# Kernel optimization log

Hardware: AMD Instinct MI355X
Metric: run time of the kernel (lower is better)

## Reference

```python
import jax, jax.numpy as jnp
import numpy as np

N = 50000; E = 400000; T = 300000; Q = 200000
F_IN = 128; H = 8; DIM = 32; D = H * DIM; NUM_RBF = 40
CENTERS = jnp.arange(0.0, 10.0, 0.25, dtype=jnp.float32)  # 40 RBF centers
BETA = 40.0  # 10 / gap


def _norm(v):
    return jnp.sqrt(jnp.sum(jnp.square(v), -1) + 1e-12)


def _rbf(d):  # d: [M] -> [M, NUM_RBF]
    return jnp.exp(-BETA * jnp.square(d[:, None] - CENTERS))


def _angle(a, m, b):  # angle at m
    u = a - m; v = b - m
    c = jnp.sum(u * v, -1) / (_norm(u) * _norm(v) + 1e-12)
    return jnp.arccos(jnp.clip(c, -1.0 + 1e-7, 1.0 - 1e-7))


def _dihedral(p0, p1, p2, p3):
    b1 = p1 - p0; b2 = p2 - p1; b3 = p3 - p2
    n1 = jnp.cross(b1, b2); n2 = jnp.cross(b2, b3)
    m1 = jnp.cross(n1, b2 / (_norm(b2)[:, None] + 1e-12))
    return jnp.arctan2(jnp.sum(m1 * n2, -1), jnp.sum(n1 * n2, -1) + 1e-12)


def _pos_encoding():  # sinusoidal PE over the length-4 [src,mid2,mid1,dst] sequence
    i = jnp.arange(0, D, 2, dtype=jnp.float32)
    div = jnp.exp(-jnp.log(10000.0) * i / D)
    ang = jnp.arange(4.0)[:, None] * div[None, :]
    pe = jnp.zeros((4, D), jnp.float32)
    return pe.at[:, 0::2].set(jnp.sin(ang)).at[:, 1::2].set(jnp.cos(ang))


def _seg_softmax(score, dst):  # softmax over irregular neighbor sets per dst node
    e = jnp.exp(score - score.max())  # global-max shift, as in original
    den = jax.ops.segment_sum(e, dst, num_segments=N)
    return e / (den[dst] + 1e-16)


def _forward(x, pos, W_src, W_dst, W_mid1, W_mid2, W_pos_bonded, b_pos_bonded,
             W_pos_unb, b_pos_unb, W_pos_unb1, b_pos_unb1, W_pos_unb2, b_pos_unb2,
             W_angle, b_angle, W_dihedral, b_dihedral, W_1hop, b_1hop, W_2hop, b_2hop,
             W_3hop, b_3hop, attn2, attn3, attn4, W_res, bias, ln_gamma, ln_beta,
             prelu_w, edge_index, triple_index, quadra_index, edge_attr):
    pe = _pos_encoding()
    src = (x @ W_src + pe[0]).reshape(N, H, DIM)
    mid2 = (x @ W_mid2 + pe[1]).reshape(N, H, DIM)
    mid1 = (x @ W_mid1 + pe[2]).reshape(N, H, DIM)
    dst = (x @ W_dst + pe[3]).reshape(N, H, DIM)

    # ---- 1-hop edge attention ----
    es, ed = edge_index[0], edge_index[1]
    d1 = _norm(pos[es] - pos[ed])
    d1c = jnp.clip(d1, 0.05, 10.0)
    bonded = jnp.stack([d1, d1 * d1], -1)  # [E,2]
    ea = edge_attr.astype(jnp.float32)[:, None]
    dmat = ((bonded * (1.0 - ea)) @ W_pos_bonded + b_pos_bonded
            + (_rbf(d1c) * ea) @ W_pos_unb + b_pos_unb).reshape(-1, H, DIM)
    a = jax.nn.leaky_relu((mid1[es] + dst[ed]) * dmat, 0.2)
    score = jnp.sum(attn2[None] * a, -1)  # [E,H]
    w = _seg_softmax(score, ed)[..., None]
    out1 = jax.ops.segment_sum(mid1[es] * w, ed, num_segments=N)

    # ---- 2-hop (angle) attention ----
    ts, tm, td = triple_index[0], triple_index[1], triple_index[2]
    d2 = jnp.clip(_norm(pos[ts] - pos[td]), 0.05, 10.0)
    dmat2 = (_rbf(d2) @ W_pos_unb1 + b_pos_unb1).reshape(-1, H, DIM)
    ang = _angle(pos[ts], pos[tm], pos[td])
    amat = (jnp.stack([ang, ang * ang], -1) @ W_angle + b_angle).reshape(-1, H, DIM)
    a = jax.nn.leaky_relu((mid2[ts] + dst[td] + mid1[tm]) * (amat + dmat2), 0.2)
    score = jnp.sum(attn3[None] * a, -1)
    w = _seg_softmax(score, td)[..., None]
    out2 = jax.ops.segment_sum(mid2[ts] * w, td, num_segments=N)

    # ---- 3-hop (dihedral) attention ----
    qs, q2, q1, qd = quadra_index[0], quadra_index[1], quadra_index[2], quadra_index[3]
    d3 = jnp.clip(_norm(pos[qs] - pos[qd]), 0.05, 10.0)
    dmat3 = (_rbf(d3) @ W_pos_unb2 + b_pos_unb2).reshape(-1, H, DIM)
    a1 = _angle(pos[qs], pos[q2], pos[q1])
    a2 = _angle(pos[q2], pos[q1], pos[qd])
    dh = _dihedral(pos[qs], pos[q2], pos[q1], pos[qd])
    feat = jnp.stack([a1, a1 * a1, a2, a2 * a2, dh, dh * dh], -1)  # [Q,6]
    hmat = (feat @ W_dihedral + b_dihedral).reshape(-1, H, DIM)
    a = jax.nn.leaky_relu((src[qs] + mid2[q2] + mid1[q1] + dst[qd]) * (hmat + dmat3), 0.2)
    score = jnp.sum(attn4[None] * a, -1)
    w = _seg_softmax(score, qd)[..., None]
    out3 = jax.ops.segment_sum(src[qs] * w, qd, num_segments=N)

    out = (out1.reshape(N, D) @ W_1hop + b_1hop
           + out2.reshape(N, D) @ W_2hop + b_2hop
           + out3.reshape(N, D) @ W_3hop + b_3hop)
    out = out + x @ W_res + bias  # residual + bias
    mu = jnp.mean(out, -1, keepdims=True)
    var = jnp.mean(jnp.square(out - mu), -1, keepdims=True)
    out = (out - mu) * jax.lax.rsqrt(var + 1e-5) * ln_gamma + ln_beta
    return jnp.where(out >= 0, out, prelu_w * out)  # PReLU


def setup_inputs():
    key = jax.random.key(0)
    ks = jax.random.split(key, 40)
    inp = {}
    inp['x'] = jax.random.normal(ks[0], (N, F_IN), jnp.float32)
    inp['pos'] = jax.random.normal(ks[1], (N, 3), jnp.float32) * 3.0
    inp['edge_index'] = jax.random.randint(ks[2], (2, E), 0, N)
    inp['triple_index'] = jax.random.randint(ks[3], (3, T), 0, N)
    inp['quadra_index'] = jax.random.randint(ks[4], (4, Q), 0, N)
    inp['edge_attr'] = jax.random.randint(ks[5], (E,), 0, 2).astype(bool)
    params = [('W_src', (F_IN, D)), ('W_dst', (F_IN, D)), ('W_mid1', (F_IN, D)),
              ('W_mid2', (F_IN, D)), ('W_pos_bonded', (2, D)), ('b_pos_bonded', (D,)),
              ('W_pos_unb', (NUM_RBF, D)), ('b_pos_unb', (D,)),
              ('W_pos_unb1', (NUM_RBF, D)), ('b_pos_unb1', (D,)),
              ('W_pos_unb2', (NUM_RBF, D)), ('b_pos_unb2', (D,)),
              ('W_angle', (2, D)), ('b_angle', (D,)),
              ('W_dihedral', (6, D)), ('b_dihedral', (D,)),
              ('W_1hop', (D, D)), ('b_1hop', (D,)),
              ('W_2hop', (D, D)), ('b_2hop', (D,)),
              ('W_3hop', (D, D)), ('b_3hop', (D,)),
              ('attn2', (H, DIM)), ('attn3', (H, DIM)), ('attn4', (H, DIM)),
              ('W_res', (F_IN, D)), ('bias', (D,))]
    for i, (nm, sh) in enumerate(params):
        inp[nm] = jax.random.normal(ks[6 + i], sh, jnp.float32) * 0.05
    inp['ln_gamma'] = jnp.ones((D,), jnp.float32)
    inp['ln_beta'] = jnp.zeros((D,), jnp.float32)
    inp['prelu_w'] = jnp.full((1,), 0.25, jnp.float32)
    return inp


def reference(x, pos, edge_index, triple_index, quadra_index, edge_attr,
              W_src, W_dst, W_mid1, W_mid2, W_pos_bonded, b_pos_bonded,
              W_pos_unb, b_pos_unb, W_pos_unb1, b_pos_unb1, W_pos_unb2, b_pos_unb2,
              W_angle, b_angle, W_dihedral, b_dihedral, W_1hop, b_1hop, W_2hop, b_2hop,
              W_3hop, b_3hop, attn2, attn3, attn4, W_res, bias, ln_gamma, ln_beta, prelu_w):
    return _forward(x, pos, W_src, W_dst, W_mid1, W_mid2, W_pos_bonded, b_pos_bonded,
                    W_pos_unb, b_pos_unb, W_pos_unb1, b_pos_unb1, W_pos_unb2, b_pos_unb2,
                    W_angle, b_angle, W_dihedral, b_dihedral, W_1hop, b_1hop, W_2hop, b_2hop,
                    W_3hop, b_3hop, attn2, attn3, attn4, W_res, bias, ln_gamma, ln_beta,
                    prelu_w, edge_index, triple_index, quadra_index, edge_attr)
```

## Files before the change

kernel.cpp:

```cpp
#include <hip/hip_runtime.h>

#define NN 50000
#define NE 400000
#define NT 300000
#define NQ 200000
#define DM 256
#define FIN 128
#define NRBF 40
#define BETA_RBF 40.0f
#define TOTALP 397569

#define WSWZ_N (56 * 16 * 64 * 8)

#define NPB1 8
#define NPB2 8
#define NPB3 16
#define NBT1 (NN / NPB1)
#define NBT2 (NN / NPB2)
#define NBT3 (NN / NPB3)
#define NBT (NBT1 + NBT2 + NBT3)

typedef unsigned int u32;
typedef unsigned short u16;
typedef __attribute__((ext_vector_type(8))) short bf16x8;
typedef __attribute__((ext_vector_type(4))) float f32x4;

static __device__ __forceinline__ float bf2f(u16 h) {
  return __uint_as_float(((u32)h) << 16);
}
static __device__ __forceinline__ u16 f2bf(float f) {
  u32 u = __float_as_uint(f);
  u32 r = (u + 0x7FFFu + ((u >> 16) & 1u)) >> 16;
  return (u16)r;
}
static __device__ __forceinline__ float4 ld4f(const float* p) {
  return *reinterpret_cast<const float4*>(p);
}
static __device__ __forceinline__ float ldsc(const void* p, int isf, size_t i) {
  return isf ? ((const float*)p)[i] : bf2f(((const u16*)p)[i]);
}
static __device__ __forceinline__ float lk(float t) { return t >= 0.f ? t : 0.2f * t; }
static __device__ __forceinline__ u32 f2o(float f) {
  u32 u = __float_as_uint(f);
  return (u & 0x80000000u) ? ~u : (u | 0x80000000u);
}

struct F3 { float x, y, z; };
static __device__ __forceinline__ F3 ldp(const float* pos, int i) {
  return F3{pos[3 * i], pos[3 * i + 1], pos[3 * i + 2]};
}
static __device__ __forceinline__ F3 sub3(F3 a, F3 b) { return F3{a.x - b.x, a.y - b.y, a.z - b.z}; }
static __device__ __forceinline__ float dot3(F3 a, F3 b) { return a.x * b.x + a.y * b.y + a.z * b.z; }
static __device__ __forceinline__ F3 cross3(F3 a, F3 b) {
  return F3{a.y * b.z - a.z * b.y, a.z * b.x - a.x * b.z, a.x * b.y - a.y * b.x};
}
static __device__ __forceinline__ float norm3(F3 v) { return sqrtf(dot3(v, v) + 1e-12f); }
static __device__ __forceinline__ float angle_at(F3 a, F3 m, F3 b) {
  F3 u = sub3(a, m), v = sub3(b, m);
  float c = dot3(u, v) / (norm3(u) * norm3(v) + 1e-12f);
  c = fminf(fmaxf(c, -1.f + 1e-7f), 1.f - 1e-7f);
  return acosf(c);
}
static __device__ __forceinline__ float dihedral_f(F3 p0, F3 p1, F3 p2, F3 p3) {
  F3 b1 = sub3(p1, p0), b2 = sub3(p2, p1), b3 = sub3(p3, p2);
  F3 n1 = cross3(b1, b2), n2 = cross3(b2, b3);
  float nb2 = norm3(b2) + 1e-12f;
  F3 b2n{b2.x / nb2, b2.y / nb2, b2.z / nb2};
  F3 m1 = cross3(n1, b2n);
  return atan2f(dot3(m1, n2), dot3(n1, n2) + 1e-12f);
}

static __device__ __forceinline__ int rbf_coef(float d, float* c) {
  int j = (int)floorf(d * 4.0f) - 3;
  j = (j < 0) ? 0 : ((j > NRBF - 8) ? (NRBF - 8) : j);
  float t0 = d - 0.25f * (float)j;
#pragma unroll
  for (int k = 0; k < 8; ++k) {
    float t = t0 - 0.25f * (float)k;
    c[k] = __expf(-BETA_RBF * t * t);
  }
  return j;
}

static __device__ __forceinline__ float4 rbf_apply(const float* __restrict__ base,
                                                   float4 c0, float4 c1, float4 dm) {
  float4 w;
  w = ld4f(base + 0 * DM);
  dm.x = fmaf(c0.x, w.x, dm.x); dm.y = fmaf(c0.x, w.y, dm.y);
  dm.z = fmaf(c0.x, w.z, dm.z); dm.w = fmaf(c0.x, w.w, dm.w);
  w = ld4f(base + 1 * DM);
  dm.x = fmaf(c0.y, w.x, dm.x); dm.y = fmaf(c0.y, w.y, dm.y);
  dm.z = fmaf(c0.y, w.z, dm.z); dm.w = fmaf(c0.y, w.w, dm.w);
  w = ld4f(base + 2 * DM);
  dm.x = fmaf(c0.z, w.x, dm.x); dm.y = fmaf(c0.z, w.y, dm.y);
  dm.z = fmaf(c0.z, w.z, dm.z); dm.w = fmaf(c0.z, w.w, dm.w);
  w = ld4f(base + 3 * DM);
  dm.x = fmaf(c0.w, w.x, dm.x); dm.y = fmaf(c0.w, w.y, dm.y);
  dm.z = fmaf(c0.w, w.z, dm.z); dm.w = fmaf(c0.w, w.w, dm.w);
  w = ld4f(base + 4 * DM);
  dm.x = fmaf(c1.x, w.x, dm.x); dm.y = fmaf(c1.x, w.y, dm.y);
  dm.z = fmaf(c1.x, w.z, dm.z); dm.w = fmaf(c1.x, w.w, dm.w);
  w = ld4f(base + 5 * DM);
  dm.x = fmaf(c1.y, w.x, dm.x); dm.y = fmaf(c1.y, w.y, dm.y);
  dm.z = fmaf(c1.y, w.z, dm.z); dm.w = fmaf(c1.y, w.w, dm.w);
  w = ld4f(base + 6 * DM);
  dm.x = fmaf(c1.z, w.x, dm.x); dm.y = fmaf(c1.z, w.y, dm.y);
  dm.z = fmaf(c1.z, w.z, dm.z); dm.w = fmaf(c1.z, w.w, dm.w);
  w = ld4f(base + 7 * DM);
  dm.x = fmaf(c1.w, w.x, dm.x); dm.y = fmaf(c1.w, w.y, dm.y);
  dm.z = fmaf(c1.w, w.z, dm.z); dm.w = fmaf(c1.w, w.w, dm.w);
  return dm;
}

static __device__ __forceinline__ ushort4 g512(const u16* p, int idx, int c4) {
  return *reinterpret_cast<const ushort4*>(p + (size_t)(u32)idx * DM + c4);
}
static __device__ __forceinline__ float4 cvt4(ushort4 v) {
  return float4{bf2f(v.x), bf2f(v.y), bf2f(v.z), bf2f(v.w)};
}

__device__ const int g_off[31] = {
  0, 32768, 65536, 98304, 131072, 131584, 131840, 142080, 142336, 152576,
  152832, 163072, 163328, 163840, 164096, 165632, 165888, 231424, 231680,
  297216, 297472, 363008, 363264, 363520, 363776, 364032, 396800, 397056,
  397312, 397568, 397569};
struct PtrTab { const void* p[30]; };

__global__ __launch_bounds__(256) void init_detect(const u32* __restrict__ aw,
                                                   const u32* __restrict__ lng,
                                                   u32* __restrict__ gmax,
                                                   int* __restrict__ flags) {
  __shared__ int s_int, s_f32, s_bf;
  if (threadIdx.x == 0) { s_int = 1; s_f32 = 1; s_bf = 1; }
  __syncthreads();
  int li = 1, lf = 1, lb = 1;
  for (int i = threadIdx.x; i < 1024; i += 256) {
    u32 w = aw[i];
    if (w > 1u) li = 0;
    if (w != 0u && w != 0x3F800000u) lf = 0;
    u32 h0 = w & 0xFFFFu, h1 = w >> 16;
    if ((h0 != 0u && h0 != 0x3F80u) || (h1 != 0u && h1 != 0x3F80u)) lb = 0;
  }
  if (!li) atomicAnd(&s_int, 0);
  if (!lf) atomicAnd(&s_f32, 0);
  if (!lb) atomicAnd(&s_bf, 0);
  __syncthreads();
  if (threadIdx.x == 0) {
    flags[0] = s_int ? 0 : (s_f32 ? 2 : (s_bf ? 3 : 1));
    flags[1] = ((lng[0] & 0xFFFFu) == 0x3F80u) ? 0 : 1;
    gmax[0] = f2o(-INFINITY);
    gmax[1] = f2o(-INFINITY);
    gmax[2] = f2o(-INFINITY);
    gmax[3] = 0u;
  }
}

__global__ __launch_bounds__(256) void convert_params(PtrTab tab,
                                                      const int* __restrict__ flags,
                                                      float* __restrict__ dst) {
  const int isf = flags[1];
  for (int i = blockIdx.x * blockDim.x + threadIdx.x; i < TOTALP;
       i += gridDim.x * blockDim.x) {
    int t = 0;
    while (i >= g_off[t + 1]) ++t;
    dst[i] = ldsc(tab.p[t], isf, i - g_off[t]);
  }
}
__global__ __launch_bounds__(256) void convert_pos(const void* __restrict__ pos,
                                                   const int* __restrict__ flags,
                                                   float* __restrict__ posf) {
  const int isf = flags[1];
  for (int i = blockIdx.x * blockDim.x + threadIdx.x; i < NN * 3;
       i += gridDim.x * blockDim.x)
    posf[i] = ldsc(pos, isf, i);
}

static __device__ __forceinline__ int read_eattr(const void* p, int flag, int e) {
  if (flag == 1) return ((const unsigned char*)p)[e];
  if (flag == 2) return (((const float*)p)[e] != 0.f);
  if (flag == 3) return (((const u16*)p)[e] != 0);
  return ((const int*)p)[e];
}

__global__ __launch_bounds__(256) void swizzle_w(const float* __restrict__ fp,
                                                 u16* __restrict__ wswz) {
  int idx = blockIdx.x * 256 + threadIdx.x;
  if (idx >= WSWZ_N) return;
  int jj = idx & 7;
  int lane = (idx >> 3) & 63;
  int nb = (idx >> 9) & 15;
  int s = idx >> 13;
  int kl = (lane >> 4) * 8 + jj;
  int col = nb * 16 + (lane & 15);
  float w;
  int lo;
  if (s < 48) {
    int sr = (s < 24) ? s : (s - 24);
    lo = (s >= 24);
    int K = sr * 32 + kl;
    int base = (K < 256) ? 165888 : ((K < 512) ? 231680 : 297472);
    w = fp[base + (K & 255) * 256 + col];
  } else {
    int sr = (s < 52) ? (s - 48) : (s - 52);
    lo = (s >= 52);
    int K = sr * 32 + kl;
    w = fp[364032 + K * 256 + col];
  }
  u16 hi = f2bf(w);
  wswz[idx] = lo ? f2bf(w - bf2f(hi)) : hi;
}

__global__ __launch_bounds__(256) void xsplit(const void* __restrict__ x,
                                              const int* __restrict__ flags,
                                              u16* __restrict__ Xs) {
  const int isf = flags[1];
  for (int i = blockIdx.x * blockDim.x + threadIdx.x; i < NN * FIN;
       i += gridDim.x * blockDim.x) {
    int n = i >> 7, k = i & 127;
    float v = ldsc(x, isf, i);
    u16 hi = f2bf(v);
    Xs[(size_t)n * 256 + k] = hi;
    Xs[(size_t)n * 256 + 128 + k] = f2bf(v - bf2f(hi));
  }
}

__global__ __launch_bounds__(256) void proj4_kernel(
    const void* __restrict__ x, const int* __restrict__ flags,
    const float* __restrict__ W0, const float* __restrict__ W1,
    const float* __restrict__ W2, const float* __restrict__ W3,
    u16* __restrict__ o0, u16* __restrict__ o1,
    u16* __restrict__ o2, u16* __restrict__ o3) {
  __shared__ float sx[16 * FIN];
  const int c = threadIdx.x;
  const int n0 = blockIdx.x * 16;
  const int isf = flags[1];
#pragma unroll
  for (int i = 0; i < 8; ++i) {
    int l = i * 256 + c;
    sx[l] = ldsc(x, isf, (size_t)n0 * FIN + l);
  }
  __syncthreads();
  float dv = expf(-logf(10000.f) * (float)(c & ~1) / 256.f);
  float p0 = (c & 1) ? cosf(0.f * dv) : sinf(0.f * dv);
  float p1 = (c & 1) ? cosf(1.f * dv) : sinf(1.f * dv);
  float p2 = (c & 1) ? cosf(2.f * dv) : sinf(2.f * dv);
  float p3 = (c & 1) ? cosf(3.f * dv) : sinf(3.f * dv);
  float a0[16], a1[16], a2[16], a3[16];
#pragma unroll
  for (int r = 0; r < 16; ++r) { a0[r] = p0; a1[r] = p1; a2[r] = p2; a3[r] = p3; }
  for (int k = 0; k < FIN; ++k) {
    float w0 = W0[k * DM + c], w1 = W1[k * DM + c];
    float w2 = W2[k * DM + c], w3 = W3[k * DM + c];
#pragma unroll
    for (int r = 0; r < 16; ++r) {
      float xr = sx[r * FIN + k];
      a0[r] = fmaf(xr, w0, a0[r]);
      a1[r] = fmaf(xr, w1, a1[r]);
      a2[r] = fmaf(xr, w2, a2[r]);
      a3[r] = fmaf(xr, w3, a3[r]);
    }
  }
#pragma unroll
  for (int r = 0; r < 16; ++r) {
    size_t off = (size_t)(n0 + r) * DM + c;
    o0[off] = f2bf(a0[r]); o1[off] = f2bf(a1[r]);
    o2[off] = f2bf(a2[r]); o3[off] = f2bf(a3[r]);
  }
}

__global__ __launch_bounds__(256) void hist_all(const int* __restrict__ ed,
                                                const int* __restrict__ td,
                                                const int* __restrict__ qd,
                                                int* __restrict__ deg) {
  const int M = NE + NT + NQ;
  for (int i = blockIdx.x * blockDim.x + threadIdx.x; i < M; i += gridDim.x * blockDim.x) {
    if (i < NE) atomicAdd(&deg[ed[i]], 1);
    else if (i < NE + NT) atomicAdd(&deg[NN + td[i - NE]], 1);
    else atomicAdd(&deg[2 * NN + qd[i - NE - NT]], 1);
  }
}
__global__ __launch_bounds__(1024) void scan_all(const int* __restrict__ degall,
                                                 int* __restrict__ offall,
                                                 int* __restrict__ curall) {
  __shared__ int part[1024];
  const int b = blockIdx.x;
  const int* deg = degall + (size_t)b * NN;
  int* off = offall + (size_t)b * (NN + 1);
  int* cur = curall + (size_t)b * NN;
  const int CH = (NN + 1023) / 1024;
  const int t = threadIdx.x;
  const int base = t * CH;
  int s = 0;
  for (int i = 0; i < CH; ++i) { int idx = base + i; if (idx < NN) s += deg[idx]; }
  part[t] = s;
  __syncthreads();
  for (int d = 1; d < 1024; d <<= 1) {
    int v = (t >= d) ? part[t - d] : 0;
    __syncthreads();
    part[t] += v;
    __syncthreads();
  }
  int run = (t == 0) ? 0 : part[t - 1];
  for (int i = 0; i < CH; ++i) {
    int idx = base + i;
    if (idx < NN) { off[idx] = run; cur[idx] = run; run += deg[idx]; }
  }
  if (t == 1023) off[NN] = run;
}
__global__ __launch_bounds__(256) void fill_all(const int* __restrict__ ed,
                                                const int* __restrict__ td,
                                                const int* __restrict__ qd,
                                                int* __restrict__ cur,
                                                int* __restrict__ eid) {
  const int M = NE + NT + NQ;
  for (int i = blockIdx.x * blockDim.x + threadIdx.x; i < M; i += gridDim.x * blockDim.x) {
    if (i < NE) {
      int p = atomicAdd(&cur[ed[i]], 1);
      eid[p] = i;
    } else if (i < NE + NT) {
      int il = i - NE;
      int p = atomicAdd(&cur[NN + td[il]], 1);
      eid[NE + p] = il;
    } else {
      int il = i - NE - NT;
      int p = atomicAdd(&cur[2 * NN + qd[il]], 1);
      eid[NE + NT + p] = il;
    }
  }
}

#define FINALIZE(node, hopoff)                                         \
  {                                                                    \
    float inv = 1.f / (den + 1e-16f);                                  \
    ushort4 o;                                                         \
    o.x = f2bf(acc.x * inv); o.y = f2bf(acc.y * inv);                  \
    o.z = f2bf(acc.z * inv); o.w = f2bf(acc.w * inv);                  \
    *reinterpret_cast<ushort4*>(Abuf + (size_t)(node) * 768 +          \
                                (hopoff) + c4) = o;                    \
    den = 0.f; mrun = -INFINITY;                                       \
    acc = float4{0.f, 0.f, 0.f, 0.f};                                  \
  }

__global__ __launch_bounds__(256, 4) void fused_score_agg(
    const float* __restrict__ pos,
    const int* __restrict__ eidx, const int* __restrict__ tdx, const int* __restrict__ qdx,
    const void* __restrict__ eattr, const int* __restrict__ flags,
    const u16* __restrict__ p_src, const u16* __restrict__ p_mid2,
    const u16* __restrict__ p_mid1, const u16* __restrict__ p_dst,
    const float* __restrict__ fp,
    const int* __restrict__ offall, const int* __restrict__ eidall,
    u32* __restrict__ gmax, u16* __restrict__ Abuf) {
  __shared__ __align__(16) float slds[4][64 * 20];
  const int lane = threadIdx.x & 63;
  float* sw = slds[threadIdx.x >> 6];
  const int c4 = lane * 4;
  const int flag = flags[0];

  for (int it = 0; it <= NBT; ++it) {
    u32 bl = 0;
    if (lane == 0) bl = atomicAdd(gmax + 3, 1u);
    u32 b = (u32)__builtin_amdgcn_readfirstlane((int)bl);
    if (b >= NBT) break;

    if (b < NBT1) {
      const int n0 = (int)b * NPB1;
      const int* offp = offall;
      const int* eidp = eidall;
      int offreg = offp[n0 + ((lane <= NPB1) ? lane : NPB1)];
      const int gs = __shfl(offreg, 0, 64);
      const int ge = __shfl(offreg, NPB1, 64);
      const float* Wu = fp + 131840;
      float4 av = ld4f(fp + 363264 + c4);
      float4 bbv = ld4f(fp + 131584 + c4), buv = ld4f(fp + 142080 + c4);
      float4 bsum{bbv.x + buv.x, bbv.y + buv.y, bbv.z + buv.z, bbv.w + buv.w};
      float4 wb0 = ld4f(fp + 131072 + c4), wb1 = ld4f(fp + 131072 + DM + c4);
      int kcur = 0;
      float mrun = -INFINITY, den = 0.f;
      float4 acc{0.f, 0.f, 0.f, 0.f};
      for (int cb = gs; cb < ge; cb += 64) {
        const int cl = (ge - cb < 64) ? (ge - cb) : 64;
        const int idx = cb + lane;
        int k = 0;
#pragma unroll
        for (int kk = 1; kk < NPB1; ++kk) {
          int v = __shfl(offreg, kk, 64);
          if (idx >= v) k = kk;
        }
        if (lane < cl) {
          int e = eidp[idx];
          int es = eidx[e];
          int ea = read_eattr(eattr, flag, e);
          F3 Ps = ldp(pos, es), Pd = ldp(pos, n0 + k);
          float d1 = norm3(sub3(Ps, Pd));
          float c[8]; int j = 0; float f0, f1;
          if (ea) {
            float dc = fminf(fmaxf(d1, 0.05f), 10.f);
            j = rbf_coef(dc, c);
            f0 = 0.f; f1 = 0.f;
          } else {
#pragma unroll
            for (int kk = 0; kk < 8; ++kk) c[kk] = 0.f;
            f0 = d1; f1 = d1 * d1;
          }
          float* sp = sw + lane * 20;
          *reinterpret_cast<int4*>(sp) = int4{es, ea, j, k};
          *reinterpret_cast<float4*>(sp + 4) = float4{c[0], c[1], c[2], c[3]};
          *reinterpret_cast<float4*>(sp + 8) = float4{c[4], c[5], c[6], c[7]};
          *reinterpret_cast<float4*>(sp + 12) = float4{f0, f1, 0.f, 0.f};
        }
        int4 I = *reinterpret_cast<const int4*>(sw);
        ushort4 gm = g512(p_mid1, I.x, c4);
        ushort4 gdd = g512(p_dst, n0 + I.w, c4);
#pragma unroll 1
        for (int e = 0; e < cl; ++e) {
          int4 In{0, 0, 0, 0};
          ushort4 gmn{0, 0, 0, 0}, gddn{0, 0, 0, 0};
          if (e + 1 < cl) {
            In = *reinterpret_cast<const int4*>(sw + (e + 1) * 20);
            gmn = g512(p_mid1, In.x, c4);
            gddn = g512(p_dst, n0 + In.w, c4);
          }
          while (kcur < I.w) { FINALIZE(n0 + kcur, 0); ++kcur; }
          const float* sp = sw + e * 20;
          float4 dm = bsum;
          if (I.y) {
            float4 cc0 = *reinterpret_cast<const float4*>(sp + 4);
            float4 cc1 = *reinterpret_cast<const float4*>(sp + 8);
            dm = rbf_apply(Wu + I.z * DM + c4, cc0, cc1, dm);
          } else {
            float4 f = *reinterpret_cast<const float4*>(sp + 12);
            dm.x = fmaf(f.x, wb0.x, fmaf(f.y, wb1.x, dm.x));
            dm.y = fmaf(f.x, wb0.y, fmaf(f.y, wb1.y, dm.y));
            dm.z = fmaf(f.x, wb0.z, fmaf(f.y, wb1.z, dm.z));
            dm.w = fmaf(f.x, wb0.w, fmaf(f.y, wb1.w, dm.w));
          }
          float4 mv = cvt4(gm), dd = cvt4(gdd);
          float t0 = lk((mv.x + dd.x) * dm.x);
          float t1 = lk((mv.y + dd.y) * dm.y);
          float t2 = lk((mv.z + dd.z) * dm.z);
          float t3 = lk((mv.w + dd.w) * dm.w);
          float part = av.x * t0 + av.y * t1 + av.z * t2 + av.w * t3;
          part += __shfl_xor(part, 1, 64);
          part += __shfl_xor(part, 2, 64);
          part += __shfl_xor(part, 4, 64);
          float mn = fmaxf(mrun, part);
          float r = __expf(mrun - mn);
          float ew = __expf(part - mn);
          den = den * r + ew;
          acc.x = fmaf(acc.x, r, ew * mv.x);
          acc.y = fmaf(acc.y, r, ew * mv.y);
          acc.z = fmaf(acc.z, r, ew * mv.z);
          acc.w = fmaf(acc.w, r, ew * mv.w);
          mrun = mn;
          I = In; gm = gmn; gdd = gddn;
        }
      }
      while (kcur < NPB1) { FINALIZE(n0 + kcur, 0); ++kcur; }
    } else if (b < NBT1 + NBT2) {
      const int n0 = ((int)b - NBT1) * NPB2;
      const int* offp = offall + (NN + 1);
      const int* eidp = eidall + NE;
      int offreg = offp[n0 + ((lane <= NPB2) ? lane : NPB2)];
      const int gs = __shfl(offreg, 0, 64);
      const int ge = __shfl(offreg, NPB2, 64);
      const float* Wu1 = fp + 142336;
      float4 av = ld4f(fp + 363520 + c4);
      float4 b1v = ld4f(fp + 152576 + c4), b2v = ld4f(fp + 163840 + c4);
      float4 bsum{b1v.x + b2v.x, b1v.y + b2v.y, b1v.z + b2v.z, b1v.w + b2v.w};
      float4 wa0 = ld4f(fp + 163328 + c4), wa1 = ld4f(fp + 163328 + DM + c4);
      int kcur = 0;
      float mrun = -INFINITY, den = 0.f;
      float4 acc{0.f, 0.f, 0.f, 0.f};
      for (int cb = gs; cb < ge; cb += 64) {
        const int cl = (ge - cb < 64) ? (ge - cb) : 64;
        const int idx = cb + lane;
        int k = 0;
#pragma unroll
        for (int kk = 1; kk < NPB2; ++kk) {
          int v = __shfl(offreg, kk, 64);
          if (idx >= v) k = kk;
        }
        if (lane < cl) {
          int t = eidp[idx];
          int ts = tdx[t], tm = tdx[NT + t];
          F3 Ps = ldp(pos, ts), Pm = ldp(pos, tm), Pd = ldp(pos, n0 + k);
          float d2 = fminf(fmaxf(norm3(sub3(Ps, Pd)), 0.05f), 10.f);
          float c[8];
          int j = rbf_coef(d2, c);
          float ang = angle_at(Ps, Pm, Pd);
          float* sp = sw + lane * 20;
          *reinterpret_cast<int4*>(sp) = int4{ts, tm, j, k};
          *reinterpret_cast<float4*>(sp + 4) = float4{c[0], c[1], c[2], c[3]};
          *reinterpret_cast<float4*>(sp + 8) = float4{c[4], c[5], c[6], c[7]};
          *reinterpret_cast<float4*>(sp + 12) = float4{ang, ang * ang, 0.f, 0.f};
        }
        int4 I = *reinterpret_cast<const int4*>(sw);
        ushort4 g0 = g512(p_mid2, I.x, c4);
        ushort4 g1 = g512(p_mid1, I.y, c4);
        ushort4 gdd = g512(p_dst, n0 + I.w, c4);
#pragma unroll 1
        for (int e = 0; e < cl; ++e) {
          int4 In{0, 0, 0, 0};
          ushort4 g0n{0, 0, 0, 0}, g1n{0, 0, 0, 0}, gddn{0, 0, 0, 0};
          if (e + 1 < cl) {
            In = *reinterpret_cast<const int4*>(sw + (e + 1) * 20);
            g0n = g512(p_mid2, In.x, c4);
            g1n = g512(p_mid1, In.y, c4);
            gddn = g512(p_dst, n0 + In.w, c4);
          }
          while (kcur < I.w) { FINALIZE(n0 + kcur, 256); ++kcur; }
          const float* sp = sw + e * 20;
          float4 cc0 = *reinterpret_cast<const float4*>(sp + 4);
          float4 cc1 = *reinterpret_cast<const float4*>(sp + 8);
          float4 f = *reinterpret_cast<const float4*>(sp + 12);
          float4 dm;
          dm.x = fmaf(f.x, wa0.x, fmaf(f.y, wa1.x, bsum.x));
          dm.y = fmaf(f.x, wa0.y, fmaf(f.y, wa1.y, bsum.y));
          dm.z = fmaf(f.x, wa0.z, fmaf(f.y, wa1.z, bsum.z));
          dm.w = fmaf(f.x, wa0.w, fmaf(f.y, wa1.w, bsum.w));
          dm = rbf_apply(Wu1 + I.z * DM + c4, cc0, cc1, dm);
          float4 v0 = cvt4(g0), v2 = cvt4(g1), dd = cvt4(gdd);
          float t0 = lk((v0.x + dd.x + v2.x) * dm.x);
          float t1 = lk((v0.y + dd.y + v2.y) * dm.y);
          float t2 = lk((v0.z + dd.z + v2.z) * dm.z);
          float t3 = lk((v0.w + dd.w + v2.w) * dm.w);
          float part = av.x * t0 + av.y * t1 + av.z * t2 + av.w * t3;
          part += __shfl_xor(part, 1, 64);
          part += __shfl_xor(part, 2, 64);
          part += __shfl_xor(part, 4, 64);
          float mn = fmaxf(mrun, part);
          float r = __expf(mrun - mn);
          float ew = __expf(part - mn);
          den = den * r + ew;
          acc.x = fmaf(acc.x, r, ew * v0.x);
          acc.y = fmaf(acc.y, r, ew * v0.y);
          acc.z = fmaf(acc.z, r, ew * v0.z);
          acc.w = fmaf(acc.w, r, ew * v0.w);
          mrun = mn;
          I = In; g0 = g0n; g1 = g1n; gdd = gddn;
        }
      }
      while (kcur < NPB2) { FINALIZE(n0 + kcur, 256); ++kcur; }
    } else {
      const int n0 = ((int)b - NBT1 - NBT2) * NPB3;
      const int* offp = offall + 2 * (NN + 1);
      const int* eidp = eidall + NE + NT;
      int offreg = offp[n0 + ((lane <= NPB3) ? lane : NPB3)];
      const int gs = __shfl(offreg, 0, 64);
      const int ge = __shfl(offreg, NPB3, 64);
      const float* Wu2 = fp + 152832;
      const float* Wd = fp + 164096;
      float4 av = ld4f(fp + 363776 + c4);
      float4 b1v = ld4f(fp + 163072 + c4), b2v = ld4f(fp + 165632 + c4);
      float4 bsum{b1v.x + b2v.x, b1v.y + b2v.y, b1v.z + b2v.z, b1v.w + b2v.w};
      float4 wd0 = ld4f(Wd + c4), wd1 = ld4f(Wd + DM + c4), wd2 = ld4f(Wd + 2 * DM + c4);
      float4 wd3 = ld4f(Wd + 3 * DM + c4), wd4 = ld4f(Wd + 4 * DM + c4), wd5 = ld4f(Wd + 5 * DM + c4);
      int kcur = 0;
      float mrun = -INFINITY, den = 0.f;
      float4 acc{0.f, 0.f, 0.f, 0.f};
      for (int cb = gs; cb < ge; cb += 64) {
        const int cl = (ge - cb < 64) ? (ge - cb) : 64;
        const int idx = cb + lane;
        int k = 0;
#pragma unroll
        for (int kk = 1; kk < NPB3; ++kk) {
          int v = __shfl(offreg, kk, 64);
          if (idx >= v) k = kk;
        }
        if (lane < cl) {
          int q = eidp[idx];
          int qs = qdx[q], q2 = qdx[NQ + q], q1 = qdx[2 * NQ + q];
          F3 P0 = ldp(pos, qs), P1 = ldp(pos, q2), P2 = ldp(pos, q1);
          F3 Pd = ldp(pos, n0 + k);
          float d3 = fminf(fmaxf(norm3(sub3(P0, Pd)), 0.05f), 10.f);
          float c[8];
          int j = rbf_coef(d3, c);
          float a1f = angle_at(P0, P1, P2);
          float a2f = angle_at(P1, P2, Pd);
          float dh = dihedral_f(P0, P1, P2, Pd);
          float* sp = sw + lane * 20;
          *reinterpret_cast<int4*>(sp) = int4{qs, q2, q1, j};
          *reinterpret_cast<float4*>(sp + 4) = float4{c[0], c[1], c[2], c[3]};
          *reinterpret_cast<float4*>(sp + 8) = float4{c[4], c[5], c[6], c[7]};
          *reinterpret_cast<float4*>(sp + 12) = float4{a1f, a1f * a1f, a2f, a2f * a2f};
          *reinterpret_cast<float4*>(sp + 16) = float4{dh, dh * dh, __int_as_float(k), 0.f};
        }
        int4 I = *reinterpret_cast<const int4*>(sw);
        float4 fb = *reinterpret_cast<const float4*>(sw + 16);
        ushort4 g0 = g512(p_src, I.x, c4), g1 = g512(p_mid2, I.y, c4);
        ushort4 g2 = g512(p_mid1, I.z, c4);
        ushort4 gdd = g512(p_dst, n0 + __float_as_int(fb.z), c4);
#pragma unroll 1
        for (int e = 0; e < cl; ++e) {
          int4 In{0, 0, 0, 0};
          float4 fbn{0.f, 0.f, 0.f, 0.f};
          ushort4 g0n{0, 0, 0, 0}, g1n{0, 0, 0, 0}, g2n{0, 0, 0, 0}, gddn{0, 0, 0, 0};
          if (e + 1 < cl) {
            In = *reinterpret_cast<const int4*>(sw + (e + 1) * 20);
            fbn = *reinterpret_cast<const float4*>(sw + (e + 1) * 20 + 16);
            g0n = g512(p_src, In.x, c4);
            g1n = g512(p_mid2, In.y, c4);
            g2n = g512(p_mid1, In.z, c4);
            gddn = g512(p_dst, n0 + __float_as_int(fbn.z), c4);
          }
          int kE = __float_as_int(fb.z);
          while (kcur < kE) { FINALIZE(n0 + kcur, 512); ++kcur; }
          const float* sp = sw + e * 20;
          float4 cc0 = *reinterpret_cast<const float4*>(sp + 4);
          float4 cc1 = *reinterpret_cast<const float4*>(sp + 8);
          float4 f = *reinterpret_cast<const float4*>(sp + 12);
          float4 dm;
          dm.x = bsum.x + f.x * wd0.x + f.y * wd1.x + f.z * wd2.x + f.w * wd3.x + fb.x * wd4.x + fb.y * wd5.x;
          dm.y = bsum.y + f.x * wd0.y + f.y * wd1.y + f.z * wd2.y + f.w * wd3.y + fb.x * wd4.y + fb.y * wd5.y;
          dm.z = bsum.z + f.x * wd0.z + f.y * wd1.z + f.z * wd2.z + f.w * wd3.z + fb.x * wd4.z + fb.y * wd5.z;
          dm.w = bsum.w + f.x * wd0.w + f.y * wd1.w + f.z * wd2.w + f.w * wd3.w + fb.x * wd4.w + fb.y * wd5.w;
          dm = rbf_apply(Wu2 + I.w * DM + c4, cc0, cc1, dm);
          float4 v0 = cvt4(g0), v1 = cvt4(g1), v2 = cvt4(g2), dd = cvt4(gdd);
          float t0 = lk((v0.x + v1.x + v2.x + dd.x) * dm.x);
          float t1 = lk((v0.y + v1.y + v2.y + dd.y) * dm.y);
          float t2 = lk((v0.z + v1.z + v2.z + dd.z) * dm.z);
          float t3 = lk((v0.w + v1.w + v2.w + dd.w) * dm.w);
          float part = av.x * t0 + av.y * t1 + av.z * t2 + av.w * t3;
          part += __shfl_xor(part, 1, 64);
          part += __shfl_xor(part, 2, 64);
          part += __shfl_xor(part, 4, 64);
          float mn = fmaxf(mrun, part);
          float r = __expf(mrun - mn);
          float ew = __expf(part - mn);
          den = den * r + ew;
          acc.x = fmaf(acc.x, r, ew * v0.x);
          acc.y = fmaf(acc.y, r, ew * v0.y);
          acc.z = fmaf(acc.z, r, ew * v0.z);
          acc.w = fmaf(acc.w, r, ew * v0.w);
          mrun = mn;
          I = In; fb = fbn; g0 = g0n; g1 = g1n; g2 = g2n; gdd = gddn;
        }
      }
      while (kcur < NPB3) { FINALIZE(n0 + kcur, 512); ++kcur; }
    }
  }
}

__global__ __launch_bounds__(256) void gemm_mfma_ln(
    const u16* __restrict__ Abuf, const u16* __restrict__ Xs,
    const u16* __restrict__ wswz, const float* __restrict__ fp,
    float* __restrict__ outp) {
  __shared__ float sS[4][32], sQ[4][32], sMu[32], sRs[32];
  const int tid = threadIdx.x;
  const int wid = tid >> 6, lane = tid & 63;
  const int g = lane >> 4, l15 = lane & 15;
  const int m0 = blockIdx.x * 32;
  const int cb = wid * 64;

  f32x4 acc[2][4];
#pragma unroll
  for (int nf = 0; nf < 4; ++nf) {
    int c = cb + nf * 16 + l15;
    float bs = fp[231424 + c] + fp[297216 + c] + fp[363008 + c] + fp[396800 + c];
    acc[0][nf] = f32x4{bs, bs, bs, bs};
    acc[1][nf] = f32x4{bs, bs, bs, bs};
  }
  int rr0 = m0 + l15; if (rr0 > NN - 1) rr0 = NN - 1;
  int rr1 = m0 + 16 + l15; if (rr1 > NN - 1) rr1 = NN - 1;
  const u16* a0p = Abuf + (size_t)rr0 * 768 + g * 8;
  const u16* a1p = Abuf + (size_t)rr1 * 768 + g * 8;
  const u16* x0p = Xs + (size_t)rr0 * 256 + g * 8;
  const u16* x1p = Xs + (size_t)rr1 * 256 + g * 8;
  const u16* wb = wswz + (size_t)(wid * 4 * 64 + lane) * 8;

#pragma unroll 2
  for (int ks = 0; ks < 24; ++ks) {
    bf16x8 a0 = *reinterpret_cast<const bf16x8*>(a0p + ks * 32);
    bf16x8 a1 = *reinterpret_cast<const bf16x8*>(a1p + ks * 32);
#pragma unroll
    for (int nf = 0; nf < 4; ++nf) {
      bf16x8 bh = *reinterpret_cast<const bf16x8*>(wb + (size_t)ks * 8192 + nf * 512);
      bf16x8 bl = *reinterpret_cast<const bf16x8*>(wb + (size_t)(ks + 24) * 8192 + nf * 512);
      acc[0][nf] = __builtin_amdgcn_mfma_f32_16x16x32_bf16(a0, bh, acc[0][nf], 0, 0, 0);
      acc[1][nf] = __builtin_amdgcn_mfma_f32_16x16x32_bf16(a1, bh, acc[1][nf], 0, 0, 0);
      acc[0][nf] = __builtin_amdgcn_mfma_f32_16x16x32_bf16(a0, bl, acc[0][nf], 0, 0, 0);
      acc[1][nf] = __builtin_amdgcn_mfma_f32_16x16x32_bf16(a1, bl, acc[1][nf], 0, 0, 0);
    }
  }
#pragma unroll
  for (int ks = 0; ks < 4; ++ks) {
    bf16x8 xh0 = *reinterpret_cast<const bf16x8*>(x0p + ks * 32);
    bf16x8 xh1 = *reinterpret_cast<const bf16x8*>(x1p + ks * 32);
    bf16x8 xl0 = *reinterpret_cast<const bf16x8*>(x0p + 128 + ks * 32);
    bf16x8 xl1 = *reinterpret_cast<const bf16x8*>(x1p + 128 + ks * 32);
#pragma unroll
    for (int nf = 0; nf < 4; ++nf) {
      bf16x8 bh = *reinterpret_cast<const bf16x8*>(wb + (size_t)(48 + ks) * 8192 + nf * 512);
      bf16x8 bl = *reinterpret_cast<const bf16x8*>(wb + (size_t)(52 + ks) * 8192 + nf * 512);
      acc[0][nf] = __builtin_amdgcn_mfma_f32_16x16x32_bf16(xh0, bh, acc[0][nf], 0, 0, 0);
      acc[1][nf] = __builtin_amdgcn_mfma_f32_16x16x32_bf16(xh1, bh, acc[1][nf], 0, 0, 0);
      acc[0][nf] = __builtin_amdgcn_mfma_f32_16x16x32_bf16(xh0, bl, acc[0][nf], 0, 0, 0);
      acc[1][nf] = __builtin_amdgcn_mfma_f32_16x16x32_bf16(xh1, bl, acc[1][nf], 0, 0, 0);
      acc[0][nf] = __builtin_amdgcn_mfma_f32_16x16x32_bf16(xl0, bh, acc[0][nf], 0, 0, 0);
      acc[1][nf] = __builtin_amdgcn_mfma_f32_16x16x32_bf16(xl1, bh, acc[1][nf], 0, 0, 0);
    }
  }

#pragma unroll
  for (int mf = 0; mf < 2; ++mf) {
#pragma unroll
    for (int reg = 0; reg < 4; ++reg) {
      float sp = acc[mf][0][reg] + acc[mf][1][reg] + acc[mf][2][reg] + acc[mf][3][reg];
      float qp = acc[mf][0][reg] * acc[mf][0][reg] + acc[mf][1][reg] * acc[mf][1][reg] +
                 acc[mf][2][reg] * acc[mf][2][reg] + acc[mf][3][reg] * acc[mf][3][reg];
      for (int m = 8; m; m >>= 1) {
        sp += __shfl_xor(sp, m, 64);
        qp += __shfl_xor(qp, m, 64);
      }
      if (l15 == 0) {
        sS[wid][mf * 16 + g * 4 + reg] = sp;
        sQ[wid][mf * 16 + g * 4 + reg] = qp;
      }
    }
  }
  __syncthreads();
  if (tid < 32) {
    float S = sS[0][tid] + sS[1][tid] + sS[2][tid] + sS[3][tid];
    float Q = sQ[0][tid] + sQ[1][tid] + sQ[2][tid] + sQ[3][tid];
    float mu = S * (1.f / 256.f);
    float var = fmaxf(Q * (1.f / 256.f) - mu * mu, 0.f);
    sMu[tid] = mu;
    sRs[tid] = rsqrtf(var + 1e-5f);
  }
  __syncthreads();
  float pw = fp[397568];
#pragma unroll
  for (int nf = 0; nf < 4; ++nf) {
    int c = cb + nf * 16 + l15;
    float gc = fp[397056 + c], bc = fp[397312 + c];
#pragma unroll
    for (int mf = 0; mf < 2; ++mf) {
#pragma unroll
      for (int reg = 0; reg < 4; ++reg) {
        int rl = mf * 16 + g * 4 + reg;
        int row = m0 + rl;
        if (row < NN) {
          float y = (acc[mf][nf][reg] - sMu[rl]) * sRs[rl] * gc + bc;
          outp[(size_t)row * 256 + c] = (y >= 0.f) ? y : pw * y;
        }
      }
    }
  }
}

extern "C" void kernel_launch(void* const* d_in, const int* in_sizes, int n_in,
                              void* d_out, int out_size, void* d_ws, size_t ws_size,
                              hipStream_t stream) {
  const void* x = d_in[0];
  const void* pos = d_in[1];
  const int* eidx = (const int*)d_in[2];
  const int* tdx = (const int*)d_in[3];
  const int* qdx = (const int*)d_in[4];
  const void* eattr = d_in[5];
  float* outp = (float*)d_out;

  u16* p_src = (u16*)d_ws;
  u16* p_mid2 = p_src + (size_t)NN * DM;
  u16* p_mid1 = p_mid2 + (size_t)NN * DM;
  u16* p_dst = p_mid1 + (size_t)NN * DM;
  u16* Abuf = p_dst + (size_t)NN * DM;
  float* posf = (float*)(Abuf + (size_t)NN * 768);
  float* fp = posf + (size_t)NN * 3;
  u16* wswz = (u16*)(fp + TOTALP + 3);
  int* deg = (int*)(fp + TOTALP + 3 + WSWZ_N / 2);
  int* off = deg + 3 * NN;
  int* cur = off + 3 * (NN + 1);
  int* eid = cur + 3 * NN;
  u32* gmax = (u32*)(eid + NE + NT + NQ);
  int* flags = (int*)(gmax + 4);
  u16* Xs = p_dst;

  const float* W_src = fp + 0;
  const float* W_dst = fp + 32768;
  const float* W_mid1 = fp + 65536;
  const float* W_mid2 = fp + 98304;

  init_detect<<<1, 256, 0, stream>>>((const u32*)eattr, (const u32*)d_in[33], gmax, flags);

  PtrTab tab;
  for (int i = 0; i < 30; ++i) tab.p[i] = d_in[6 + i];
  convert_params<<<512, 256, 0, stream>>>(tab, flags, fp);
  convert_pos<<<587, 256, 0, stream>>>(pos, flags, posf);
  swizzle_w<<<WSWZ_N / 256, 256, 0, stream>>>(fp, wswz);

  proj4_kernel<<<NN / 16, 256, 0, stream>>>(x, flags, W_src, W_mid2, W_mid1, W_dst,
                                            p_src, p_mid2, p_mid1, p_dst);

  hipMemsetAsync(deg, 0, (size_t)3 * NN * 4, stream);
  hist_all<<<1024, 256, 0, stream>>>(eidx + NE, tdx + 2 * NT, qdx + 3 * NQ, deg);
  scan_all<<<3, 1024, 0, stream>>>(deg, off, cur);
  fill_all<<<1024, 256, 0, stream>>>(eidx + NE, tdx + 2 * NT, qdx + 3 * NQ, cur, eid);

  fused_score_agg<<<2048, 256, 0, stream>>>(posf, eidx, tdx, qdx, eattr, flags,
                                            p_src, p_mid2, p_mid1, p_dst, fp,
                                            off, eid, gmax, Abuf);

  xsplit<<<2048, 256, 0, stream>>>(x, flags, Xs);

  gemm_mfma_ln<<<(NN + 31) / 32, 256, 0, stream>>>(Abuf, Xs, wswz, fp, outp);
}
```

Measured before the change: 1.250 ms.

## Move the four input projections onto bf16 MFMA with split-precision weights

Replaces the scalar FP32 FMA projection kernel for src/mid2/mid1/dst with an MFMA kernel. It uses hi/lo bf16 splitting of both x and the weights (three products) to stay close to fp32 accuracy. A new swizzle kernel pre-packs the projection weights into MFMA fragment order. xsplit now runs before the projection and writes to a dedicated buffer so its output can be reused by the final GEMM. This cuts ALU time for a 50000x128x1024 GEMM, at the cost of an extra workspace buffer and a small extra prep launch.

```diff
diff --git a/kernel.cpp b/kernel.cpp
--- a/kernel.cpp
+++ b/kernel.cpp
@@ -11,6 +11,7 @@
 #define TOTALP 397569
 
 #define WSWZ_N (56 * 16 * 64 * 8)
+#define PSWZ_N (4 * 2 * 4 * 16 * 64 * 8)
 
 #define NPB1 8
 #define NPB2 8
@@ -210,6 +211,24 @@
   wswz[idx] = lo ? f2bf(w - bf2f(hi)) : hi;
 }
 
+__global__ __launch_bounds__(256) void swizzle_pw(const float* __restrict__ fp,
+                                                  u16* __restrict__ pswz) {
+  int idx = blockIdx.x * 256 + threadIdx.x;
+  if (idx >= PSWZ_N) return;
+  int jj = idx & 7;
+  int lane = (idx >> 3) & 63;
+  int nb = (idx >> 9) & 15;
+  int ks = (idx >> 13) & 3;
+  int hilo = (idx >> 15) & 1;
+  int mat = idx >> 16;
+  const int mb[4] = {0, 98304, 65536, 32768};
+  int K = ks * 32 + (lane >> 4) * 8 + jj;
+  int col = nb * 16 + (lane & 15);
+  float w = fp[mb[mat] + K * 256 + col];
+  u16 hi = f2bf(w);
+  pswz[idx] = hilo ? f2bf(w - bf2f(hi)) : hi;
+}
+
 __global__ __launch_bounds__(256) void xsplit(const void* __restrict__ x,
                                               const int* __restrict__ flags,
                                               u16* __restrict__ Xs) {
@@ -224,47 +243,72 @@
   }
 }
 
-__global__ __launch_bounds__(256) void proj4_kernel(
-    const void* __restrict__ x, const int* __restrict__ flags,
-    const float* __restrict__ W0, const float* __restrict__ W1,
-    const float* __restrict__ W2, const float* __restrict__ W3,
+__global__ __launch_bounds__(256) void proj_mfma(
+    const u16* __restrict__ Xs, const u16* __restrict__ pswz,
     u16* __restrict__ o0, u16* __restrict__ o1,
     u16* __restrict__ o2, u16* __restrict__ o3) {
-  __shared__ float sx[16 * FIN];
-  const int c = threadIdx.x;
-  const int n0 = blockIdx.x * 16;
-  const int isf = flags[1];
-#pragma unroll
-  for (int i = 0; i < 8; ++i) {
-    int l = i * 256 + c;
-    sx[l] = ldsc(x, isf, (size_t)n0 * FIN + l);
-  }
-  __syncthreads();
-  float dv = expf(-logf(10000.f) * (float)(c & ~1) / 256.f);
-  float p0 = (c & 1) ? cosf(0.f * dv) : sinf(0.f * dv);
-  float p1 = (c & 1) ? cosf(1.f * dv) : sinf(1.f * dv);
-  float p2 = (c & 1) ? cosf(2.f * dv) : sinf(2.f * dv);
-  float p3 = (c & 1) ? cosf(3.f * dv) : sinf(3.f * dv);
-  float a0[16], a1[16], a2[16], a3[16];
-#pragma unroll
-  for (int r = 0; r < 16; ++r) { a0[r] = p0; a1[r] = p1; a2[r] = p2; a3[r] = p3; }
-  for (int k = 0; k < FIN; ++k) {
-    float w0 = W0[k * DM + c], w1 = W1[k * DM + c];
-    float w2 = W2[k * DM + c], w3 = W3[k * DM + c];
-#pragma unroll
-    for (int r = 0; r < 16; ++r) {
-      float xr = sx[r * FIN + k];
-      a0[r] = fmaf(xr, w0, a0[r]);
-      a1[r] = fmaf(xr, w1, a1[r]);
-      a2[r] = fmaf(xr, w2, a2[r]);
-      a3[r] = fmaf(xr, w3, a3[r]);
+  const int tid = threadIdx.x;
+  const int wid = tid >> 6, lane = tid & 63;
+  const int g = lane >> 4, l15 = lane & 15;
+  const int m0 = blockIdx.x * 32;
+  const int cb = wid * 64;
+
+  int rr0 = m0 + l15; if (rr0 > NN - 1) rr0 = NN - 1;
+  int rr1 = m0 + 16 + l15; if (rr1 > NN - 1) rr1 = NN - 1;
+  const u16* x0p = Xs + (size_t)rr0 * 256 + g * 8;
+  const u16* x1p = Xs + (size_t)rr1 * 256 + g * 8;
+
+  bf16x8 xh0[4], xh1[4], xl0[4], xl1[4];
+#pragma unroll
+  for (int ks = 0; ks < 4; ++ks) {
+    xh0[ks] = *reinterpret_cast<const bf16x8*>(x0p + ks * 32);
+    xh1[ks] = *reinterpret_cast<const bf16x8*>(x1p + ks * 32);
+    xl0[ks] = *reinterpret_cast<const bf16x8*>(x0p + 128 + ks * 32);
+    xl1[ks] = *reinterpret_cast<const bf16x8*>(x1p + 128 + ks * 32);
+  }
+
+  u16* const outs[4] = {o0, o1, o2, o3};
+#pragma unroll 1
+  for (int mat = 0; mat < 4; ++mat) {
+    f32x4 acc[2][4];
+#pragma unroll
+    for (int nf = 0; nf < 4; ++nf) {
+      int c = cb + nf * 16 + l15;
+      float dv = expf(-logf(10000.f) * (float)(c & ~1) / 256.f);
+      float ang = (float)mat * dv;
+      float p = (c & 1) ? cosf(ang) : sinf(ang);
+      acc[0][nf] = f32x4{p, p, p, p};
+      acc[1][nf] = f32x4{p, p, p, p};
     }
-  }
-#pragma unroll
-  for (int r = 0; r < 16; ++r) {
-    size_t off = (size_t)(n0 + r) * DM + c;
-    o0[off] = f2bf(a0[r]); o1[off] = f2bf(a1[r]);
-    o2[off] = f2bf(a2[r]); o3[off] = f2bf(a3[r]);
+    const u16* wbm = pswz + (size_t)mat * 65536 + (size_t)lane * 8;
+#pragma unroll
+    for (int ks = 0; ks < 4; ++ks) {
+#pragma unroll
+      for (int nf = 0; nf < 4; ++nf) {
+        const u16* bbase = wbm + (size_t)ks * 8192 + (wid * 4 + nf) * 512;
+        bf16x8 bh = *reinterpret_cast<const bf16x8*>(bbase);
+        bf16x8 bl = *reinterpret_cast<const bf16x8*>(bbase + 32768);
+        acc[0][nf] = __builtin_amdgcn_mfma_f32_16x16x32_bf16(xh0[ks], bh, acc[0][nf], 0, 0, 0);
+        acc[1][nf] = __builtin_amdgcn_mfma_f32_16x16x32_bf16(xh1[ks], bh, acc[1][nf], 0, 0, 0);
+        acc[0][nf] = __builtin_amdgcn_mfma_f32_16x16x32_bf16(xh0[ks], bl, acc[0][nf], 0, 0, 0);
+        acc[1][nf] = __builtin_amdgcn_mfma_f32_16x16x32_bf16(xh1[ks], bl, acc[1][nf], 0, 0, 0);
+        acc[0][nf] = __builtin_amdgcn_mfma_f32_16x16x32_bf16(xl0[ks], bh, acc[0][nf], 0, 0, 0);
+        acc[1][nf] = __builtin_amdgcn_mfma_f32_16x16x32_bf16(xl1[ks], bh, acc[1][nf], 0, 0, 0);
+      }
+    }
+    u16* op = outs[mat];
+#pragma unroll
+    for (int nf = 0; nf < 4; ++nf) {
+      int c = cb + nf * 16 + l15;
+#pragma unroll
+      for (int mf = 0; mf < 2; ++mf) {
+#pragma unroll
+        for (int reg = 0; reg < 4; ++reg) {
+          int row = m0 + mf * 16 + g * 4 + reg;
+          if (row < NN) op[(size_t)row * 256 + c] = f2bf(acc[mf][nf][reg]);
+        }
+      }
+    }
   }
 }
 
@@ -764,21 +808,17 @@
   u16* p_mid1 = p_mid2 + (size_t)NN * DM;
   u16* p_dst = p_mid1 + (size_t)NN * DM;
   u16* Abuf = p_dst + (size_t)NN * DM;
-  float* posf = (float*)(Abuf + (size_t)NN * 768);
+  u16* Xs = Abuf + (size_t)NN * 768;
+  float* posf = (float*)(Xs + (size_t)NN * 256);
   float* fp = posf + (size_t)NN * 3;
   u16* wswz = (u16*)(fp + TOTALP + 3);
-  int* deg = (int*)(fp + TOTALP + 3 + WSWZ_N / 2);
+  u16* pswz = wswz + WSWZ_N;
+  int* deg = (int*)(pswz + PSWZ_N);
   int* off = deg + 3 * NN;
   int* cur = off + 3 * (NN + 1);
   int* eid = cur + 3 * NN;
   u32* gmax = (u32*)(eid + NE + NT + NQ);
   int* flags = (int*)(gmax + 4);
-  u16* Xs = p_dst;
-
-  const float* W_src = fp + 0;
-  const float* W_dst = fp + 32768;
-  const float* W_mid1 = fp + 65536;
-  const float* W_mid2 = fp + 98304;
 
   init_detect<<<1, 256, 0, stream>>>((const u32*)eattr, (const u32*)d_in[33], gmax, flags);
 
@@ -787,9 +827,11 @@
   convert_params<<<512, 256, 0, stream>>>(tab, flags, fp);
   convert_pos<<<587, 256, 0, stream>>>(pos, flags, posf);
   swizzle_w<<<WSWZ_N / 256, 256, 0, stream>>>(fp, wswz);
-
-  proj4_kernel<<<NN / 16, 256, 0, stream>>>(x, flags, W_src, W_mid2, W_mid1, W_dst,
-                                            p_src, p_mid2, p_mid1, p_dst);
+  swizzle_pw<<<PSWZ_N / 256, 256, 0, stream>>>(fp, pswz);
+
+  xsplit<<<2048, 256, 0, stream>>>(x, flags, Xs);
+
+  proj_mfma<<<(NN + 31) / 32, 256, 0, stream>>>(Xs, pswz, p_src, p_mid2, p_mid1, p_dst);
 
   hipMemsetAsync(deg, 0, (size_t)3 * NN * 4, stream);
   hist_all<<<1024, 256, 0, stream>>>(eidx + NE, tdx + 2 * NT, qdx + 3 * NQ, deg);
@@ -800,7 +842,5 @@
                                             p_src, p_mid2, p_mid1, p_dst, fp,
                                             off, eid, gmax, Abuf);
 
-  xsplit<<<2048, 256, 0, stream>>>(x, flags, Xs);
-
   gemm_mfma_ln<<<(NN + 31) / 32, 256, 0, stream>>>(Abuf, Xs, wswz, fp, outp);
 }
```

Result: faster. 1.215 ms (-2.8%).
